# Optimization experiments

Hardware: AMD Instinct MI355X
Metric: run time of the kernel (lower is better)

Reference implementation:

```python
import jax, jax.numpy as jnp
import numpy as np

B, D, O, E = 8192, 1024, 1024, 8

def setup_inputs() -> dict:
    key = jax.random.key(0)
    ks = jax.random.split(key, 5)
    s = 1.0 / np.sqrt(D)
    return {
        "x": jax.random.normal(ks[0], (B, D), dtype=jnp.float32),
        "Wg": jax.random.uniform(ks[1], (D, E), jnp.float32, -s, s),
        "bg": jax.random.uniform(ks[2], (E,), jnp.float32, -s, s),
        "We": jax.random.uniform(ks[3], (E, D, O), jnp.float32, -s, s),
        "be": jax.random.uniform(ks[4], (E, O), jnp.float32, -s, s),
    }

def reference(x, Wg, bg, We, be):
    # gating: [B, E], softmax over experts (dim=1)
    gates = jax.nn.softmax(x @ Wg + bg, axis=1)
    # dense expert outputs: [B, E, O] (single batched GEMM over all experts)
    expert_out = jnp.einsum('bd,edo->beo', x, We) + be[None, :, :]
    # softmax-weighted combine (bmm of [B,1,E] @ [B,E,O] -> [B,O])
    return jnp.einsum('be,beo->bo', gates, expert_out)
```

## Files before the change

### kernel.cpp

```cpp
#include <hip/hip_runtime.h>
#include <hip/hip_bf16.h>
#include <stdint.h>

#define B_SZ 8192
#define D_SZ 1024
#define O_SZ 1024
#define E_SZ 8

#define BM 256
#define BN 128
#define BK 64
#define NT 128

typedef __bf16 bf16_t;
typedef __bf16 bf16x8 __attribute__((ext_vector_type(8)));
typedef __bf16 bf16x4 __attribute__((ext_vector_type(4)));
typedef float  f32x4  __attribute__((ext_vector_type(4)));

__global__ __launch_bounds__(256) void prep_kernel(
    const float* __restrict__ x, const float* __restrict__ Wg,
    const float* __restrict__ bg, const float* __restrict__ We,
    float* __restrict__ gates, bf16_t* __restrict__ xb,
    bf16_t* __restrict__ wet) {
  __shared__ float tile[64][65];
  const int bid = blockIdx.x;
  if (bid < 2048) {
    const int w = threadIdx.x >> 6, lane = threadIdx.x & 63;
    const int b = bid * 4 + w;
    const float4* xr = (const float4*)(x + (size_t)b * D_SZ);
    bf16x4* xbr = (bf16x4*)(xb + (size_t)b * D_SZ);
    float acc[8];
#pragma unroll
    for (int e = 0; e < 8; ++e) acc[e] = 0.f;
#pragma unroll 1
    for (int it = 0; it < 4; ++it) {
      int d4 = it * 64 + lane;
      float4 v = xr[d4];
      bf16x4 ob;
      ob[0] = (bf16_t)v.x; ob[1] = (bf16_t)v.y;
      ob[2] = (bf16_t)v.z; ob[3] = (bf16_t)v.w;
      xbr[d4] = ob;
      const float4* wr = (const float4*)(Wg + (size_t)d4 * 32);
      float xs[4] = {v.x, v.y, v.z, v.w};
#pragma unroll
      for (int rr = 0; rr < 4; ++rr) {
        float4 wa = wr[rr * 2], wb = wr[rr * 2 + 1];
        acc[0] += xs[rr] * wa.x; acc[1] += xs[rr] * wa.y;
        acc[2] += xs[rr] * wa.z; acc[3] += xs[rr] * wa.w;
        acc[4] += xs[rr] * wb.x; acc[5] += xs[rr] * wb.y;
        acc[6] += xs[rr] * wb.z; acc[7] += xs[rr] * wb.w;
      }
    }
#pragma unroll
    for (int off = 32; off >= 1; off >>= 1) {
#pragma unroll
      for (int e = 0; e < 8; ++e) acc[e] += __shfl_xor(acc[e], off, 64);
    }
    if (lane == 0) {
#pragma unroll
      for (int e = 0; e < 8; ++e) acc[e] += bg[e];
      float m = acc[0];
#pragma unroll
      for (int e = 1; e < 8; ++e) m = fmaxf(m, acc[e]);
      float s = 0.f, ex[8];
#pragma unroll
      for (int e = 0; e < 8; ++e) { ex[e] = __expf(acc[e] - m); s += ex[e]; }
      float inv = 1.0f / s;
      float* gr = gates + (size_t)b * 8;
#pragma unroll
      for (int e = 0; e < 8; ++e) gr[e] = ex[e] * inv;
    }
  } else {
    const int bt = bid - 2048;
    const int e = bt >> 8;
    const int d0 = ((bt >> 4) & 15) * 64, o0 = (bt & 15) * 64;
    const int tx = threadIdx.x & 63, ty = threadIdx.x >> 6;
    const float* src = We + (size_t)e * D_SZ * O_SZ;
#pragma unroll
    for (int i = 0; i < 16; ++i) {
      int d = ty + i * 4;
      tile[d][tx] = src[(size_t)(d0 + d) * O_SZ + o0 + tx];
    }
    __syncthreads();
    bf16_t* dst = wet + (size_t)e * O_SZ * D_SZ;
#pragma unroll
    for (int i = 0; i < 16; ++i) {
      int o = ty + i * 4;
      dst[(size_t)(o0 + o) * D_SZ + d0 + tx] = (bf16_t)tile[tx][o];
    }
  }
}

__device__ __forceinline__ void gl16(const bf16_t* g, const bf16_t* l) {
  __builtin_amdgcn_global_load_lds(
      (const __attribute__((address_space(1))) void*)g,
      (__attribute__((address_space(3))) void*)l, 16, 0, 0);
}

__global__ __launch_bounds__(512, 2) void moe_gemm(
    const bf16_t* __restrict__ xb,
    const bf16_t* __restrict__ wet,
    const float* __restrict__ gates,
    const float* __restrict__ be,
    float* __restrict__ out)
{
  __shared__ bf16_t lA[3][BM * BK];
  __shared__ bf16_t lB[3][BN * BK];
  __shared__ float  lG[BM * 9];
  __shared__ float  lBe[E_SZ * BN];

  const int tid = threadIdx.x;
  const int w = tid >> 6, lane = tid & 63;

  const int flat = blockIdx.x + (blockIdx.y << 3);
  const int xcd = flat & 7, slot = flat >> 3;
  const int bt = (xcd << 2) + (slot & 3);
  const int ot = slot >> 2;
  const int b0 = bt * BM;
  const int o0 = ot * BN;

  const int wm = (w >> 1) * 64, wn = (w & 1) * 64;
  const int m16 = lane & 15, q = lane >> 4;

  {
    float4 g4 = ((const float4*)(gates + (size_t)b0 * 8))[tid];
    int gr = tid >> 1, gc = (tid & 1) * 4;
    lG[gr * 9 + gc + 0] = g4.x; lG[gr * 9 + gc + 1] = g4.y;
    lG[gr * 9 + gc + 2] = g4.z; lG[gr * 9 + gc + 3] = g4.w;
#pragma unroll
    for (int p = 0; p < 2; ++p) {
      int idx = tid + p * 512;
      lBe[idx] = be[(size_t)(idx >> 7) * O_SZ + o0 + (idx & 127)];
    }
  }

  const bf16_t* aptr[4]; int aoffL[4];
#pragma unroll
  for (int j = 0; j < 4; ++j) {
    int g0 = w * 64 + 512 * j;
    int row = (g0 >> 3) + (lane >> 3);
    int ls = (lane & 7) ^ (row & 7);
    aptr[j] = xb + (size_t)(b0 + row) * D_SZ + ls * 8;
    aoffL[j] = g0 * 8;
  }
  const bf16_t* bptr[2]; int boffL[2];
#pragma unroll
  for (int j = 0; j < 2; ++j) {
    int g0 = w * 64 + 512 * j;
    int row = (g0 >> 3) + (lane >> 3);
    int ls = (lane & 7) ^ (row & 7);
    bptr[j] = wet + (size_t)(o0 + row) * D_SZ + ls * 8;
    boffL[j] = g0 * 8;
  }

  const int xk = m16 & 7;
  const int offA0 = (wm + m16) * 128 + ((q ^ xk) << 4);
  const int offA1 = (wm + m16) * 128 + (((4 | q) ^ xk) << 4);
  const int offB0 = (wn + m16) * 128 + ((q ^ xk) << 4);
  const int offB1 = (wn + m16) * 128 + (((4 | q) ^ xk) << 4);

#define STAGE(t_, buf_) do {                                                   \
    const int kk_ = ((t_) & 15) << 6;                                          \
    const size_t eo_ = (((size_t)((t_) >> 4)) << 20) + kk_;                    \
    _Pragma("unroll")                                                          \
    for (int js = 0; js < 4; ++js) gl16(aptr[js] + kk_, &lA[buf_][0] + aoffL[js]); \
    _Pragma("unroll")                                                          \
    for (int js = 0; js < 2; ++js) gl16(bptr[js] + eo_, &lB[buf_][0] + boffL[js]); \
  } while (0)

  f32x4 acc[4][4], outAcc[4][4];
#pragma unroll
  for (int i = 0; i < 4; ++i)
#pragma unroll
    for (int j = 0; j < 4; ++j) {
      acc[i][j] = f32x4{0.f, 0.f, 0.f, 0.f};
      outAcc[i][j] = f32x4{0.f, 0.f, 0.f, 0.f};
    }

  STAGE(0, 0);
  STAGE(1, 1);
  asm volatile("s_waitcnt lgkmcnt(0)" ::: "memory");

#define BODY(cur_) do {                                                        \
    const char* la_ = (const char*)(&lA[cur_][0]);                             \
    const char* lb_ = (const char*)(&lB[cur_][0]);                             \
    bf16x8 a_[4], b_[4];                                                       \
    _Pragma("unroll")                                                          \
    for (int j = 0; j < 4; ++j) b_[j] = *(const bf16x8*)(lb_ + offB0 + j * 2048); \
    _Pragma("unroll")                                                          \
    for (int i = 0; i < 4; ++i) a_[i] = *(const bf16x8*)(la_ + offA0 + i * 2048); \
    __builtin_amdgcn_s_setprio(1);                                             \
    _Pragma("unroll")                                                          \
    for (int i = 0; i < 4; ++i)                                                \
      _Pragma("unroll")                                                        \
      for (int j = 0; j < 4; ++j)                                              \
        acc[i][j] = __builtin_amdgcn_mfma_f32_16x16x32_bf16(                   \
            a_[i], b_[j], acc[i][j], 0, 0, 0);                                 \
    __builtin_amdgcn_s_setprio(0);                                             \
    _Pragma("unroll")                                                          \
    for (int j = 0; j < 4; ++j) b_[j] = *(const bf16x8*)(lb_ + offB1 + j * 2048); \
    _Pragma("unroll")                                                          \
    for (int i = 0; i < 4; ++i) a_[i] = *(const bf16x8*)(la_ + offA1 + i * 2048); \
    __builtin_amdgcn_s_setprio(1);                                             \
    _Pragma("unroll")                                                          \
    for (int i = 0; i < 4; ++i)                                                \
      _Pragma("unroll")                                                        \
      for (int j = 0; j < 4; ++j)                                              \
        acc[i][j] = __builtin_amdgcn_mfma_f32_16x16x32_bf16(                   \
            a_[i], b_[j], acc[i][j], 0, 0, 0);                                 \
    __builtin_amdgcn_s_setprio(0);                                             \
  } while (0)

#define COMBINE(e_) do {                                                       \
    float bec_[4];                                                             \
    _Pragma("unroll")                                                          \
    for (int j = 0; j < 4; ++j) bec_[j] = lBe[(e_) * BN + wn + j * 16 + m16];  \
    _Pragma("unroll")                                                          \
    for (int i = 0; i < 4; ++i) {                                              \
      _Pragma("unroll")                                                        \
      for (int rg = 0; rg < 4; ++rg) {                                         \
        float gv = lG[(wm + i * 16 + q * 4 + rg) * 9 + (e_)];                  \
        _Pragma("unroll")                                                      \
        for (int j = 0; j < 4; ++j) {                                          \
          outAcc[i][j][rg] += gv * (acc[i][j][rg] + bec_[j]);                  \
          acc[i][j][rg] = 0.f;                                                 \
        }                                                                      \
      }                                                                        \
    }                                                                          \
  } while (0)

#define STEP_S(t_, cur_, nb_) do {                                             \
    asm volatile("s_waitcnt vmcnt(6)" ::: "memory");                           \
    __builtin_amdgcn_s_barrier();                                              \
    asm volatile("" ::: "memory");                                             \
    STAGE((t_) + 2, nb_);                                                      \
    BODY(cur_);                                                                \
    if (((t_) & 15) == 15) COMBINE((t_) >> 4);                                 \
  } while (0)

#pragma unroll 1
  for (int t3 = 0; t3 < 126; t3 += 3) {
    STEP_S(t3 + 0, 0, 2);
    STEP_S(t3 + 1, 1, 0);
    STEP_S(t3 + 2, 2, 1);
  }
  asm volatile("s_waitcnt vmcnt(6)" ::: "memory");
  __builtin_amdgcn_s_barrier();
  asm volatile("" ::: "memory");
  BODY(0);
  asm volatile("s_waitcnt vmcnt(0)" ::: "memory");
  __builtin_amdgcn_s_barrier();
  asm volatile("" ::: "memory");
  BODY(1);
  COMBINE(7);

#pragma unroll
  for (int i = 0; i < 4; ++i)
#pragma unroll
    for (int rg = 0; rg < 4; ++rg) {
      float* orow = out + (size_t)(b0 + wm + i * 16 + q * 4 + rg) * O_SZ
                    + o0 + wn + m16;
#pragma unroll
      for (int j = 0; j < 4; ++j) orow[j * 16] = outAcc[i][j][rg];
    }
}

extern "C" void kernel_launch(void* const* d_in, const int* in_sizes, int n_in,
                              void* d_out, int out_size, void* d_ws, size_t ws_size,
                              hipStream_t stream) {
  const float* x  = (const float*)d_in[0];
  const float* Wg = (const float*)d_in[1];
  const float* bg = (const float*)d_in[2];
  const float* We = (const float*)d_in[3];
  const float* be = (const float*)d_in[4];
  float* out = (float*)d_out;

  char* ws = (char*)d_ws;
  float*  gates = (float*)ws;
  bf16_t* xb    = (bf16_t*)(ws + (1 << 18));
  bf16_t* wet   = (bf16_t*)(ws + (1 << 18) + (1 << 24));

  prep_kernel<<<4096, 256, 0, stream>>>(x, Wg, bg, We, gates, xb, wet);
  moe_gemm<<<dim3(O_SZ / BN, B_SZ / BM), 512, 0, stream>>>(xb, wet, gates, be, out);
}
```

Baseline: 256.9 us.

## Use 4 waves per block with 64x128 warp tiles and staggered K-halves

Halves the GEMM block from 8 waves to 4, giving each wave a 64x128 output tile (4x8 MFMA fragments) instead of 64x64, so each LDS A/B fragment load feeds more MFMAs. Odd and even waves process the two K halves in opposite order to spread LDS bank and read traffic. Each thread issues twice as many global-to-LDS loads per stage, with the vmcnt wait adjusted to match. The cost is roughly double the accumulator registers per thread and fewer waves to hide latency, with launch bounds changed to (256,1).

```diff
diff --git a/kernel.cpp b/kernel.cpp
--- a/kernel.cpp
+++ b/kernel.cpp
@@ -97,7 +97,7 @@
       (__attribute__((address_space(3))) void*)l, 16, 0, 0);
 }
 
-__global__ __launch_bounds__(512, 2) void moe_gemm(
+__global__ __launch_bounds__(256, 1) void moe_gemm(
     const bf16_t* __restrict__ xb,
     const bf16_t* __restrict__ wet,
     const float* __restrict__ gates,
@@ -119,34 +119,38 @@
   const int b0 = bt * BM;
   const int o0 = ot * BN;
 
-  const int wm = (w >> 1) * 64, wn = (w & 1) * 64;
+  const int wm = w * 64;
   const int m16 = lane & 15, q = lane >> 4;
 
   {
-    float4 g4 = ((const float4*)(gates + (size_t)b0 * 8))[tid];
-    int gr = tid >> 1, gc = (tid & 1) * 4;
-    lG[gr * 9 + gc + 0] = g4.x; lG[gr * 9 + gc + 1] = g4.y;
-    lG[gr * 9 + gc + 2] = g4.z; lG[gr * 9 + gc + 3] = g4.w;
 #pragma unroll
     for (int p = 0; p < 2; ++p) {
-      int idx = tid + p * 512;
+      int idx = tid + 256 * p;
+      float4 g4 = ((const float4*)(gates + (size_t)b0 * 8))[idx];
+      int gr = idx >> 1, gc = (idx & 1) * 4;
+      lG[gr * 9 + gc + 0] = g4.x; lG[gr * 9 + gc + 1] = g4.y;
+      lG[gr * 9 + gc + 2] = g4.z; lG[gr * 9 + gc + 3] = g4.w;
+    }
+#pragma unroll
+    for (int p = 0; p < 4; ++p) {
+      int idx = tid + 256 * p;
       lBe[idx] = be[(size_t)(idx >> 7) * O_SZ + o0 + (idx & 127)];
     }
   }
 
-  const bf16_t* aptr[4]; int aoffL[4];
-#pragma unroll
-  for (int j = 0; j < 4; ++j) {
-    int g0 = w * 64 + 512 * j;
+  const bf16_t* aptr[8]; int aoffL[8];
+#pragma unroll
+  for (int j = 0; j < 8; ++j) {
+    int g0 = w * 64 + 256 * j;
     int row = (g0 >> 3) + (lane >> 3);
     int ls = (lane & 7) ^ (row & 7);
     aptr[j] = xb + (size_t)(b0 + row) * D_SZ + ls * 8;
     aoffL[j] = g0 * 8;
   }
-  const bf16_t* bptr[2]; int boffL[2];
-#pragma unroll
-  for (int j = 0; j < 2; ++j) {
-    int g0 = w * 64 + 512 * j;
+  const bf16_t* bptr[4]; int boffL[4];
+#pragma unroll
+  for (int j = 0; j < 4; ++j) {
+    int g0 = w * 64 + 256 * j;
     int row = (g0 >> 3) + (lane >> 3);
     int ls = (lane & 7) ^ (row & 7);
     bptr[j] = wet + (size_t)(o0 + row) * D_SZ + ls * 8;
@@ -156,23 +160,23 @@
   const int xk = m16 & 7;
   const int offA0 = (wm + m16) * 128 + ((q ^ xk) << 4);
   const int offA1 = (wm + m16) * 128 + (((4 | q) ^ xk) << 4);
-  const int offB0 = (wn + m16) * 128 + ((q ^ xk) << 4);
-  const int offB1 = (wn + m16) * 128 + (((4 | q) ^ xk) << 4);
+  const int offB0 = m16 * 128 + ((q ^ xk) << 4);
+  const int offB1 = m16 * 128 + (((4 | q) ^ xk) << 4);
 
 #define STAGE(t_, buf_) do {                                                   \
     const int kk_ = ((t_) & 15) << 6;                                          \
     const size_t eo_ = (((size_t)((t_) >> 4)) << 20) + kk_;                    \
     _Pragma("unroll")                                                          \
-    for (int js = 0; js < 4; ++js) gl16(aptr[js] + kk_, &lA[buf_][0] + aoffL[js]); \
-    _Pragma("unroll")                                                          \
-    for (int js = 0; js < 2; ++js) gl16(bptr[js] + eo_, &lB[buf_][0] + boffL[js]); \
-  } while (0)
-
-  f32x4 acc[4][4], outAcc[4][4];
+    for (int js = 0; js < 8; ++js) gl16(aptr[js] + kk_, &lA[buf_][0] + aoffL[js]); \
+    _Pragma("unroll")                                                          \
+    for (int js = 0; js < 4; ++js) gl16(bptr[js] + eo_, &lB[buf_][0] + boffL[js]); \
+  } while (0)
+
+  f32x4 acc[4][8], outAcc[4][8];
 #pragma unroll
   for (int i = 0; i < 4; ++i)
 #pragma unroll
-    for (int j = 0; j < 4; ++j) {
+    for (int j = 0; j < 8; ++j) {
       acc[i][j] = f32x4{0.f, 0.f, 0.f, 0.f};
       outAcc[i][j] = f32x4{0.f, 0.f, 0.f, 0.f};
     }
@@ -181,47 +185,45 @@
   STAGE(1, 1);
   asm volatile("s_waitcnt lgkmcnt(0)" ::: "memory");
 
-#define BODY(cur_) do {                                                        \
+#define HALF(cur_, OA_, OB_) do {                                              \
     const char* la_ = (const char*)(&lA[cur_][0]);                             \
     const char* lb_ = (const char*)(&lB[cur_][0]);                             \
-    bf16x8 a_[4], b_[4];                                                       \
-    _Pragma("unroll")                                                          \
-    for (int j = 0; j < 4; ++j) b_[j] = *(const bf16x8*)(lb_ + offB0 + j * 2048); \
-    _Pragma("unroll")                                                          \
-    for (int i = 0; i < 4; ++i) a_[i] = *(const bf16x8*)(la_ + offA0 + i * 2048); \
+    bf16x8 a_[4], b_[8];                                                       \
+    _Pragma("unroll")                                                          \
+    for (int j = 0; j < 8; ++j) b_[j] = *(const bf16x8*)(lb_ + (OB_) + j * 2048); \
+    _Pragma("unroll")                                                          \
+    for (int i = 0; i < 4; ++i) a_[i] = *(const bf16x8*)(la_ + (OA_) + i * 2048); \
     __builtin_amdgcn_s_setprio(1);                                             \
     _Pragma("unroll")                                                          \
     for (int i = 0; i < 4; ++i)                                                \
       _Pragma("unroll")                                                        \
-      for (int j = 0; j < 4; ++j)                                              \
+      for (int j = 0; j < 8; ++j)                                              \
         acc[i][j] = __builtin_amdgcn_mfma_f32_16x16x32_bf16(                   \
             a_[i], b_[j], acc[i][j], 0, 0, 0);                                 \
     __builtin_amdgcn_s_setprio(0);                                             \
-    _Pragma("unroll")                                                          \
-    for (int j = 0; j < 4; ++j) b_[j] = *(const bf16x8*)(lb_ + offB1 + j * 2048); \
-    _Pragma("unroll")                                                          \
-    for (int i = 0; i < 4; ++i) a_[i] = *(const bf16x8*)(la_ + offA1 + i * 2048); \
-    __builtin_amdgcn_s_setprio(1);                                             \
-    _Pragma("unroll")                                                          \
-    for (int i = 0; i < 4; ++i)                                                \
-      _Pragma("unroll")                                                        \
-      for (int j = 0; j < 4; ++j)                                              \
-        acc[i][j] = __builtin_amdgcn_mfma_f32_16x16x32_bf16(                   \
-            a_[i], b_[j], acc[i][j], 0, 0, 0);                                 \
-    __builtin_amdgcn_s_setprio(0);                                             \
+  } while (0)
+
+#define BODY(cur_) do {                                                        \
+    if ((w & 1) == 0) {                                                        \
+      HALF(cur_, offA0, offB0);                                                \
+      HALF(cur_, offA1, offB1);                                                \
+    } else {                                                                   \
+      HALF(cur_, offA1, offB1);                                                \
+      HALF(cur_, offA0, offB0);                                                \
+    }                                                                          \
   } while (0)
 
 #define COMBINE(e_) do {                                                       \
-    float bec_[4];                                                             \
-    _Pragma("unroll")                                                          \
-    for (int j = 0; j < 4; ++j) bec_[j] = lBe[(e_) * BN + wn + j * 16 + m16];  \
+    float bec_[8];                                                             \
+    _Pragma("unroll")                                                          \
+    for (int j = 0; j < 8; ++j) bec_[j] = lBe[(e_) * BN + j * 16 + m16];       \
     _Pragma("unroll")                                                          \
     for (int i = 0; i < 4; ++i) {                                              \
       _Pragma("unroll")                                                        \
       for (int rg = 0; rg < 4; ++rg) {                                         \
         float gv = lG[(wm + i * 16 + q * 4 + rg) * 9 + (e_)];                  \
         _Pragma("unroll")                                                      \
-        for (int j = 0; j < 4; ++j) {                                          \
+        for (int j = 0; j < 8; ++j) {                                          \
           outAcc[i][j][rg] += gv * (acc[i][j][rg] + bec_[j]);                  \
           acc[i][j][rg] = 0.f;                                                 \
         }                                                                      \
@@ -230,7 +232,7 @@
   } while (0)
 
 #define STEP_S(t_, cur_, nb_) do {                                             \
-    asm volatile("s_waitcnt vmcnt(6)" ::: "memory");                           \
+    asm volatile("s_waitcnt vmcnt(12)" ::: "memory");                          \
     __builtin_amdgcn_s_barrier();                                              \
     asm volatile("" ::: "memory");                                             \
     STAGE((t_) + 2, nb_);                                                      \
@@ -244,7 +246,7 @@
     STEP_S(t3 + 1, 1, 0);
     STEP_S(t3 + 2, 2, 1);
   }
-  asm volatile("s_waitcnt vmcnt(6)" ::: "memory");
+  asm volatile("s_waitcnt vmcnt(12)" ::: "memory");
   __builtin_amdgcn_s_barrier();
   asm volatile("" ::: "memory");
   BODY(0);
@@ -259,9 +261,9 @@
 #pragma unroll
     for (int rg = 0; rg < 4; ++rg) {
       float* orow = out + (size_t)(b0 + wm + i * 16 + q * 4 + rg) * O_SZ
-                    + o0 + wn + m16;
-#pragma unroll
-      for (int j = 0; j < 4; ++j) orow[j * 16] = outAcc[i][j][rg];
+                    + o0 + m16;
+#pragma unroll
+      for (int j = 0; j < 8; ++j) orow[j * 16] = outAcc[i][j][rg];
     }
 }
 
@@ -281,5 +283,5 @@
   bf16_t* wet   = (bf16_t*)(ws + (1 << 18) + (1 << 24));
 
   prep_kernel<<<4096, 256, 0, stream>>>(x, Wg, bg, We, gates, xb, wet);
-  moe_gemm<<<dim3(O_SZ / BN, B_SZ / BM), 512, 0, stream>>>(xb, wet, gates, be, out);
-}
+  moe_gemm<<<dim3(O_SZ / BN, B_SZ / BM), 256, 0, stream>>>(xb, wet, gates, be, out);
+}
```

New measurement: 736.8 us. 2.87x slower.

## Split K across wave pairs and fold gate combine via ratio rescaling

Applied to the files above, without the earlier changes.

Each wave now computes a 128x64 tile over half of each K-step (intra-block split-K across wave pairs), so it holds one 8x4 accumulator set instead of separate acc and outAcc arrays. The gate-weighted combine becomes a running rescale of the accumulator by g[e]/g[e+1] at each expert boundary, which removes the second accumulator and the per-expert zeroing. The two K-halves are reduced through LDS scratch at the end, which costs an extra barrier and extra LDS traffic. The gate-ratio trick divides by gate values, which can lose precision when a gate is very small.

```diff
diff --git a/kernel.cpp b/kernel.cpp
--- a/kernel.cpp
+++ b/kernel.cpp
@@ -104,10 +104,11 @@
     const float* __restrict__ be,
     float* __restrict__ out)
 {
-  __shared__ bf16_t lA[3][BM * BK];
-  __shared__ bf16_t lB[3][BN * BK];
-  __shared__ float  lG[BM * 9];
-  __shared__ float  lBe[E_SZ * BN];
+  __shared__ __align__(16) char smem[160768];
+  bf16_t* lA  = (bf16_t*)smem;
+  bf16_t* lB  = (bf16_t*)(smem + 147456 - 49152);
+  float*  lGr = (float*)(smem + 147456);
+  float*  lBe = (float*)(smem + 156672);
 
   const int tid = threadIdx.x;
   const int w = tid >> 6, lane = tid & 63;
@@ -119,19 +120,25 @@
   const int b0 = bt * BM;
   const int o0 = ot * BN;
 
-  const int wm = (w >> 1) * 64, wn = (w & 1) * 64;
   const int m16 = lane & 15, q = lane >> 4;
-
-  {
-    float4 g4 = ((const float4*)(gates + (size_t)b0 * 8))[tid];
-    int gr = tid >> 1, gc = (tid & 1) * 4;
-    lG[gr * 9 + gc + 0] = g4.x; lG[gr * 9 + gc + 1] = g4.y;
-    lG[gr * 9 + gc + 2] = g4.z; lG[gr * 9 + gc + 3] = g4.w;
-#pragma unroll
-    for (int p = 0; p < 2; ++p) {
-      int idx = tid + p * 512;
-      lBe[idx] = be[(size_t)(idx >> 7) * O_SZ + o0 + (idx & 127)];
-    }
+  const int mrow = (w >> 2) << 7;
+  const int ncol = ((w >> 1) & 1) << 6;
+  const int kh4  = (w & 1) << 2;
+
+  if (tid < 256) {
+    const float4* g4 = (const float4*)(gates + (size_t)(b0 + tid) * 8);
+    float4 ga = g4[0], gb = g4[1];
+    float g[8] = {ga.x, ga.y, ga.z, ga.w, gb.x, gb.y, gb.z, gb.w};
+    float* r = lGr + tid * 9;
+#pragma unroll
+    for (int e = 0; e < 7; ++e) r[e] = g[e] / g[e + 1];
+    r[7] = g[7];
+  } else {
+    int s = tid - 256;
+    const int e = s >> 5, c = (s & 31) * 4;
+    float4 v = *(const float4*)(be + (size_t)e * O_SZ + o0 + c);
+    float* d = lBe + e * BN + c;
+    d[0] = v.x; d[1] = v.y; d[2] = v.z; d[3] = v.w;
   }
 
   const bf16_t* aptr[4]; int aoffL[4];
@@ -154,77 +161,60 @@
   }
 
   const int xk = m16 & 7;
-  const int offA0 = (wm + m16) * 128 + ((q ^ xk) << 4);
-  const int offA1 = (wm + m16) * 128 + (((4 | q) ^ xk) << 4);
-  const int offB0 = (wn + m16) * 128 + ((q ^ xk) << 4);
-  const int offB1 = (wn + m16) * 128 + (((4 | q) ^ xk) << 4);
+  const int gsel = ((kh4 | q) ^ xk) << 4;
+  const int offA = (mrow + m16) * 128 + gsel;
+  const int offB = (ncol + m16) * 128 + gsel;
 
 #define STAGE(t_, buf_) do {                                                   \
     const int kk_ = ((t_) & 15) << 6;                                          \
     const size_t eo_ = (((size_t)((t_) >> 4)) << 20) + kk_;                    \
     _Pragma("unroll")                                                          \
-    for (int js = 0; js < 4; ++js) gl16(aptr[js] + kk_, &lA[buf_][0] + aoffL[js]); \
-    _Pragma("unroll")                                                          \
-    for (int js = 0; js < 2; ++js) gl16(bptr[js] + eo_, &lB[buf_][0] + boffL[js]); \
-  } while (0)
-
-  f32x4 acc[4][4], outAcc[4][4];
-#pragma unroll
-  for (int i = 0; i < 4; ++i)
-#pragma unroll
-    for (int j = 0; j < 4; ++j) {
-      acc[i][j] = f32x4{0.f, 0.f, 0.f, 0.f};
-      outAcc[i][j] = f32x4{0.f, 0.f, 0.f, 0.f};
-    }
+    for (int js = 0; js < 4; ++js) gl16(aptr[js] + kk_, lA + (buf_) * 16384 + aoffL[js]); \
+    _Pragma("unroll")                                                          \
+    for (int js = 0; js < 2; ++js) gl16(bptr[js] + eo_, lB + (buf_) * 8192 + boffL[js]); \
+  } while (0)
+
+  f32x4 acc[8][4];
+#pragma unroll
+  for (int i = 0; i < 8; ++i)
+#pragma unroll
+    for (int j = 0; j < 4; ++j) acc[i][j] = f32x4{0.f, 0.f, 0.f, 0.f};
 
   STAGE(0, 0);
   STAGE(1, 1);
   asm volatile("s_waitcnt lgkmcnt(0)" ::: "memory");
 
 #define BODY(cur_) do {                                                        \
-    const char* la_ = (const char*)(&lA[cur_][0]);                             \
-    const char* lb_ = (const char*)(&lB[cur_][0]);                             \
-    bf16x8 a_[4], b_[4];                                                       \
-    _Pragma("unroll")                                                          \
-    for (int j = 0; j < 4; ++j) b_[j] = *(const bf16x8*)(lb_ + offB0 + j * 2048); \
-    _Pragma("unroll")                                                          \
-    for (int i = 0; i < 4; ++i) a_[i] = *(const bf16x8*)(la_ + offA0 + i * 2048); \
+    const char* la_ = (const char*)lA + (cur_) * 32768;                        \
+    const char* lb_ = (const char*)lB + (cur_) * 16384;                        \
+    bf16x8 a_[8], b_[4];                                                       \
+    _Pragma("unroll")                                                          \
+    for (int j = 0; j < 4; ++j) b_[j] = *(const bf16x8*)(lb_ + offB + j * 2048); \
+    _Pragma("unroll")                                                          \
+    for (int i = 0; i < 8; ++i) a_[i] = *(const bf16x8*)(la_ + offA + i * 2048); \
     __builtin_amdgcn_s_setprio(1);                                             \
     _Pragma("unroll")                                                          \
-    for (int i = 0; i < 4; ++i)                                                \
+    for (int i = 0; i < 8; ++i)                                                \
       _Pragma("unroll")                                                        \
       for (int j = 0; j < 4; ++j)                                              \
         acc[i][j] = __builtin_amdgcn_mfma_f32_16x16x32_bf16(                   \
             a_[i], b_[j], acc[i][j], 0, 0, 0);                                 \
     __builtin_amdgcn_s_setprio(0);                                             \
-    _Pragma("unroll")                                                          \
-    for (int j = 0; j < 4; ++j) b_[j] = *(const bf16x8*)(lb_ + offB1 + j * 2048); \
-    _Pragma("unroll")                                                          \
-    for (int i = 0; i < 4; ++i) a_[i] = *(const bf16x8*)(la_ + offA1 + i * 2048); \
-    __builtin_amdgcn_s_setprio(1);                                             \
-    _Pragma("unroll")                                                          \
-    for (int i = 0; i < 4; ++i)                                                \
-      _Pragma("unroll")                                                        \
-      for (int j = 0; j < 4; ++j)                                              \
-        acc[i][j] = __builtin_amdgcn_mfma_f32_16x16x32_bf16(                   \
-            a_[i], b_[j], acc[i][j], 0, 0, 0);                                 \
-    __builtin_amdgcn_s_setprio(0);                                             \
-  } while (0)
-
-#define COMBINE(e_) do {                                                       \
+  } while (0)
+
+#define BOUND(e_) do {                                                         \
     float bec_[4];                                                             \
     _Pragma("unroll")                                                          \
-    for (int j = 0; j < 4; ++j) bec_[j] = lBe[(e_) * BN + wn + j * 16 + m16];  \
-    _Pragma("unroll")                                                          \
-    for (int i = 0; i < 4; ++i) {                                              \
+    for (int j = 0; j < 4; ++j)                                                \
+      bec_[j] = (w & 1) ? 0.f : lBe[(e_) * BN + ncol + j * 16 + m16];          \
+    _Pragma("unroll")                                                          \
+    for (int i = 0; i < 8; ++i) {                                              \
       _Pragma("unroll")                                                        \
       for (int rg = 0; rg < 4; ++rg) {                                         \
-        float gv = lG[(wm + i * 16 + q * 4 + rg) * 9 + (e_)];                  \
+        float rt = lGr[(mrow + i * 16 + q * 4 + rg) * 9 + (e_)];               \
         _Pragma("unroll")                                                      \
-        for (int j = 0; j < 4; ++j) {                                          \
-          outAcc[i][j][rg] += gv * (acc[i][j][rg] + bec_[j]);                  \
-          acc[i][j][rg] = 0.f;                                                 \
-        }                                                                      \
+        for (int j = 0; j < 4; ++j)                                            \
+          acc[i][j][rg] = (acc[i][j][rg] + bec_[j]) * rt;                      \
       }                                                                        \
     }                                                                          \
   } while (0)
@@ -235,7 +225,7 @@
     asm volatile("" ::: "memory");                                             \
     STAGE((t_) + 2, nb_);                                                      \
     BODY(cur_);                                                                \
-    if (((t_) & 15) == 15) COMBINE((t_) >> 4);                                 \
+    if (((t_) & 15) == 15) BOUND((t_) >> 4);                                   \
   } while (0)
 
 #pragma unroll 1
@@ -252,17 +242,35 @@
   __builtin_amdgcn_s_barrier();
   asm volatile("" ::: "memory");
   BODY(1);
-  COMBINE(7);
-
-#pragma unroll
-  for (int i = 0; i < 4; ++i)
-#pragma unroll
-    for (int rg = 0; rg < 4; ++rg) {
-      float* orow = out + (size_t)(b0 + wm + i * 16 + q * 4 + rg) * O_SZ
-                    + o0 + wn + m16;
-#pragma unroll
-      for (int j = 0; j < 4; ++j) orow[j * 16] = outAcc[i][j][rg];
-    }
+  BOUND(7);
+
+  asm volatile("s_waitcnt lgkmcnt(0)" ::: "memory");
+  __builtin_amdgcn_s_barrier();
+  float* scr = (float*)smem + (size_t)(w >> 1) * (128 * 65);
+  if (w & 1) {
+#pragma unroll
+    for (int i = 0; i < 8; ++i)
+#pragma unroll
+      for (int rg = 0; rg < 4; ++rg) {
+        float* sr = scr + (i * 16 + q * 4 + rg) * 65 + m16;
+#pragma unroll
+        for (int j = 0; j < 4; ++j) sr[j * 16] = acc[i][j][rg];
+      }
+  }
+  asm volatile("s_waitcnt lgkmcnt(0)" ::: "memory");
+  __builtin_amdgcn_s_barrier();
+  if (!(w & 1)) {
+#pragma unroll
+    for (int i = 0; i < 8; ++i)
+#pragma unroll
+      for (int rg = 0; rg < 4; ++rg) {
+        int r = i * 16 + q * 4 + rg;
+        const float* sr = scr + r * 65 + m16;
+        float* orow = out + (size_t)(b0 + mrow + r) * O_SZ + o0 + ncol + m16;
+#pragma unroll
+        for (int j = 0; j < 4; ++j) orow[j * 16] = acc[i][j][rg] + sr[j * 16];
+      }
+  }
 }
 
 extern "C" void kernel_launch(void* const* d_in, const int* in_sizes, int n_in,
```

Measured after the change: 403.3 us. +57.0%, slower.

## Load B operand directly from global into registers, bypassing LDS

Applied to the files above, without the earlier changes.

Removes the LDS staging buffer for the expert weight tile and loads each wave's B fragments straight from global memory into registers at the start of every k-step. This drops the LDS footprint and the LDS reads for B, and the vmcnt wait thresholds are adjusted to match. The B loads are issued in the same step that consumes them, so they are not prefetched and their global-memory latency is exposed to the MFMAs. Waves that share B columns also fetch the same data redundantly.

```diff
diff --git a/kernel.cpp b/kernel.cpp
--- a/kernel.cpp
+++ b/kernel.cpp
@@ -105,7 +105,6 @@
     float* __restrict__ out)
 {
   __shared__ bf16_t lA[3][BM * BK];
-  __shared__ bf16_t lB[3][BN * BK];
   __shared__ float  lG[BM * 9];
   __shared__ float  lBe[E_SZ * BN];
 
@@ -143,29 +142,31 @@
     aptr[j] = xb + (size_t)(b0 + row) * D_SZ + ls * 8;
     aoffL[j] = g0 * 8;
   }
-  const bf16_t* bptr[2]; int boffL[2];
-#pragma unroll
-  for (int j = 0; j < 2; ++j) {
-    int g0 = w * 64 + 512 * j;
-    int row = (g0 >> 3) + (lane >> 3);
-    int ls = (lane & 7) ^ (row & 7);
-    bptr[j] = wet + (size_t)(o0 + row) * D_SZ + ls * 8;
-    boffL[j] = g0 * 8;
-  }
 
   const int xk = m16 & 7;
   const int offA0 = (wm + m16) * 128 + ((q ^ xk) << 4);
   const int offA1 = (wm + m16) * 128 + (((4 | q) ^ xk) << 4);
-  const int offB0 = (wn + m16) * 128 + ((q ^ xk) << 4);
-  const int offB1 = (wn + m16) * 128 + (((4 | q) ^ xk) << 4);
+
+  int bvoff[4];
+#pragma unroll
+  for (int j = 0; j < 4; ++j) bvoff[j] = (wn + j * 16 + m16) * D_SZ + q * 8;
+
+  bf16x8 bfr[4][2];
+
+#define LOADB(t_) do {                                                         \
+    const bf16_t* bsrc_ = wet + (size_t)o0 * D_SZ +                            \
+        (((size_t)((t_) >> 4)) << 20) + (((t_) & 15) << 6);                    \
+    _Pragma("unroll")                                                          \
+    for (int j = 0; j < 4; ++j) {                                              \
+      bfr[j][0] = *(const bf16x8*)(bsrc_ + bvoff[j]);                          \
+      bfr[j][1] = *(const bf16x8*)(bsrc_ + bvoff[j] + 32);                     \
+    }                                                                          \
+  } while (0)
 
 #define STAGE(t_, buf_) do {                                                   \
     const int kk_ = ((t_) & 15) << 6;                                          \
-    const size_t eo_ = (((size_t)((t_) >> 4)) << 20) + kk_;                    \
     _Pragma("unroll")                                                          \
     for (int js = 0; js < 4; ++js) gl16(aptr[js] + kk_, &lA[buf_][0] + aoffL[js]); \
-    _Pragma("unroll")                                                          \
-    for (int js = 0; js < 2; ++js) gl16(bptr[js] + eo_, &lB[buf_][0] + boffL[js]); \
   } while (0)
 
   f32x4 acc[4][4], outAcc[4][4];
@@ -183,10 +184,7 @@
 
 #define BODY(cur_) do {                                                        \
     const char* la_ = (const char*)(&lA[cur_][0]);                             \
-    const char* lb_ = (const char*)(&lB[cur_][0]);                             \
-    bf16x8 a_[4], b_[4];                                                       \
-    _Pragma("unroll")                                                          \
-    for (int j = 0; j < 4; ++j) b_[j] = *(const bf16x8*)(lb_ + offB0 + j * 2048); \
+    bf16x8 a_[4];                                                              \
     _Pragma("unroll")                                                          \
     for (int i = 0; i < 4; ++i) a_[i] = *(const bf16x8*)(la_ + offA0 + i * 2048); \
     __builtin_amdgcn_s_setprio(1);                                             \
@@ -195,10 +193,8 @@
       _Pragma("unroll")                                                        \
       for (int j = 0; j < 4; ++j)                                              \
         acc[i][j] = __builtin_amdgcn_mfma_f32_16x16x32_bf16(                   \
-            a_[i], b_[j], acc[i][j], 0, 0, 0);                                 \
+            a_[i], bfr[j][0], acc[i][j], 0, 0, 0);                             \
     __builtin_amdgcn_s_setprio(0);                                             \
-    _Pragma("unroll")                                                          \
-    for (int j = 0; j < 4; ++j) b_[j] = *(const bf16x8*)(lb_ + offB1 + j * 2048); \
     _Pragma("unroll")                                                          \
     for (int i = 0; i < 4; ++i) a_[i] = *(const bf16x8*)(la_ + offA1 + i * 2048); \
     __builtin_amdgcn_s_setprio(1);                                             \
@@ -207,7 +203,7 @@
       _Pragma("unroll")                                                        \
       for (int j = 0; j < 4; ++j)                                              \
         acc[i][j] = __builtin_amdgcn_mfma_f32_16x16x32_bf16(                   \
-            a_[i], b_[j], acc[i][j], 0, 0, 0);                                 \
+            a_[i], bfr[j][1], acc[i][j], 0, 0, 0);                             \
     __builtin_amdgcn_s_setprio(0);                                             \
   } while (0)
 
@@ -230,9 +226,10 @@
   } while (0)
 
 #define STEP_S(t_, cur_, nb_) do {                                             \
-    asm volatile("s_waitcnt vmcnt(6)" ::: "memory");                           \
+    asm volatile("s_waitcnt vmcnt(4)" ::: "memory");                           \
     __builtin_amdgcn_s_barrier();                                              \
     asm volatile("" ::: "memory");                                             \
+    LOADB(t_);                                                                 \
     STAGE((t_) + 2, nb_);                                                      \
     BODY(cur_);                                                                \
     if (((t_) & 15) == 15) COMBINE((t_) >> 4);                                 \
@@ -244,13 +241,15 @@
     STEP_S(t3 + 1, 1, 0);
     STEP_S(t3 + 2, 2, 1);
   }
-  asm volatile("s_waitcnt vmcnt(6)" ::: "memory");
+  asm volatile("s_waitcnt vmcnt(4)" ::: "memory");
   __builtin_amdgcn_s_barrier();
   asm volatile("" ::: "memory");
+  LOADB(126);
   BODY(0);
   asm volatile("s_waitcnt vmcnt(0)" ::: "memory");
   __builtin_amdgcn_s_barrier();
   asm volatile("" ::: "memory");
+  LOADB(127);
   BODY(1);
   COMBINE(7);
 
```

Result: slower. 459.0 us (+78.6%).
